# Kernel tuning notes

Measured on AMD Instinct MI355X. Metric: run time of the kernel, lower is better.

## Reference

```python
import jax, jax.numpy as jnp
import numpy as np

D_X, N_LAYERS, N_HEADS, D_OUT = 1024, 4, 16, 1024
D_H = D_X // N_HEADS
LN_EPS = 1e-5


def _layernorm(x, g, b):
    mu = jnp.mean(x, axis=-1, keepdims=True)
    var = jnp.var(x, axis=-1, keepdims=True)
    return (x - mu) * jax.lax.rsqrt(var + LN_EPS) * g + b


def setup_inputs() -> dict:
    key = jax.random.key(0)
    ks = jax.random.split(key, 12)
    s = 0.02
    inp = {
        "x": jax.random.normal(ks[0], (4, 1024, D_X), dtype=jnp.float32),
        # per-layer, per-head K/V projections (Q is unused by the original math)
        "Wk": jax.random.normal(ks[1], (N_LAYERS, N_HEADS, D_X, D_H), dtype=jnp.float32) * s,
        "bk": jnp.zeros((N_LAYERS, N_HEADS, D_H), dtype=jnp.float32),
        "Wv": jax.random.normal(ks[2], (N_LAYERS, N_HEADS, D_X, D_H), dtype=jnp.float32) * s,
        "bv": jnp.zeros((N_LAYERS, N_HEADS, D_H), dtype=jnp.float32),
        # per-layer FFN linear
        "Wl": jax.random.normal(ks[3], (N_LAYERS, D_X, D_X), dtype=jnp.float32) * s,
        "bl": jnp.zeros((N_LAYERS, D_X), dtype=jnp.float32),
        # per-layer LayerNorm params
        "g1": jnp.ones((N_LAYERS, D_X), dtype=jnp.float32),
        "b1": jnp.zeros((N_LAYERS, D_X), dtype=jnp.float32),
        "g2": jnp.ones((N_LAYERS, D_X), dtype=jnp.float32),
        "b2": jnp.zeros((N_LAYERS, D_X), dtype=jnp.float32),
        # output projection
        "Wo": jax.random.normal(ks[4], (D_X, D_OUT), dtype=jnp.float32) * s,
        "bo": jnp.zeros((D_OUT,), dtype=jnp.float32),
    }
    return inp


def reference(x, Wk, bk, Wv, bv, Wl, bl, g1, b1, g2, b2, Wo, bo):
    B, S, _ = x.shape
    scale = 1.0 / np.sqrt(D_H).astype(np.float32)
    for l in range(N_LAYERS):
        # batched across heads instead of the original per-head Python loop
        K = jnp.einsum("bsd,hdk->bhsk", x, Wk[l]) + bk[l][None, :, None, :]
        V = jnp.einsum("bsd,hdk->bhsk", x, Wv[l]) + bv[l][None, :, None, :]
        # faithful quirk: logits = K @ V^T (Q is never used in the source)
        logits = jnp.einsum("bhsk,bhtk->bhst", K, V) * scale
        attn = jnp.einsum("bhst,bhtk->bhsk", jax.nn.softmax(logits, axis=-1), V)
        attn = attn.transpose(0, 2, 1, 3).reshape(B, S, D_X)  # concat heads
        x = _layernorm(x + attn, g1[l], b1[l])
        ff = jax.nn.relu(jnp.einsum("bsd,de->bse", x, Wl[l]) + bl[l])
        x = _layernorm(x + ff, g2[l], b2[l])
    return jnp.einsum("bsd,do->bso", x, Wo) + bo
```

## Files before the change

### kernel.cpp

```cpp
#include <hip/hip_runtime.h>

typedef unsigned short u16;
typedef unsigned int u32;
typedef __attribute__((ext_vector_type(4))) float f32x4;
typedef __attribute__((ext_vector_type(8))) short short8;

#if __has_builtin(__builtin_amdgcn_exp2f)
#define EXP2(x) __builtin_amdgcn_exp2f(x)
#else
#define EXP2(x) exp2f(x)
#endif

#define SCALEK 0.18033688011112042f

__device__ __forceinline__ u16 f2b(float f) {
    unsigned u = __float_as_uint(f);
    u += 0x7fff + ((u >> 16) & 1);
    return (u16)(u >> 16);
}
__device__ __forceinline__ float b2f(u16 v) {
    return __uint_as_float(((unsigned)v) << 16);
}
__device__ __forceinline__ int swz(int byteoff) {
    return byteoff ^ (((byteoff >> 7) & 7) << 4);
}
__device__ __forceinline__ int swzV(int byteoff) {
    return byteoff ^ (((byteoff >> 8) & 7) << 4);
}
__device__ __forceinline__ void gl16(const u16* g, u16* l) {
    __builtin_amdgcn_global_load_lds(
        (const __attribute__((address_space(1))) unsigned*)(g),
        (__attribute__((address_space(3))) unsigned*)(l), 16, 0, 0);
}
__device__ __forceinline__ u32 cvtpk(float lo, float hi) {
    u32 r;
    asm("v_cvt_pk_bf16_f32 %0, %1, %2" : "=v"(r) : "v"(lo), "v"(hi));
    return r;
}
__device__ __forceinline__ void plswap(u32& a, u32& b) {
    asm("v_permlane32_swap_b32 %0, %1" : "+v"(a), "+v"(b));
    asm("v_permlane16_swap_b32 %0, %1" : "+v"(a), "+v"(b));
}
__device__ __forceinline__ void up8(uint4 u, float* v) {
    v[0] = b2f((u16)u.x); v[1] = b2f((u16)(u.x >> 16));
    v[2] = b2f((u16)u.y); v[3] = b2f((u16)(u.y >> 16));
    v[4] = b2f((u16)u.z); v[5] = b2f((u16)(u.z >> 16));
    v[6] = b2f((u16)u.w); v[7] = b2f((u16)(u.w >> 16));
}
#define MFMA16(a, b, c) __builtin_amdgcn_mfma_f32_16x16x32_bf16((a), (b), (c), 0, 0, 0)

__global__ __launch_bounds__(256) void pack_wkv_t(const float* __restrict__ W,
                                                  u16* __restrict__ out, int voff) {
    __shared__ float tile[32][33];
    int z = blockIdx.z; int l = z >> 4, h = z & 15;
    const float* ip = W + (size_t)z * 1024 * 64;
    u16* op = out + (size_t)l * 2048 * 1024 + (size_t)(voff + h * 64) * 1024;
    int tx = threadIdx.x & 31, ty = threadIdx.x >> 5;
    int d0 = blockIdx.y * 32, k0 = blockIdx.x * 32;
#pragma unroll
    for (int j = 0; j < 32; j += 8)
        tile[ty + j][tx] = ip[(size_t)(d0 + ty + j) * 64 + k0 + tx];
    __syncthreads();
#pragma unroll
    for (int j = 0; j < 32; j += 8)
        op[(size_t)(k0 + ty + j) * 1024 + d0 + tx] = f2b(tile[tx][ty + j]);
}

__global__ __launch_bounds__(256) void transpose_cvt(const float* __restrict__ in,
                                                     u16* __restrict__ out, int R, int C) {
    __shared__ float tile[32][33];
    const float* ip = in + (size_t)blockIdx.z * R * C;
    u16* op = out + (size_t)blockIdx.z * R * C;
    int tx = threadIdx.x & 31, ty = threadIdx.x >> 5;
    int r0 = blockIdx.y * 32, c0 = blockIdx.x * 32;
#pragma unroll
    for (int j = 0; j < 32; j += 8)
        tile[ty + j][tx] = ip[(size_t)(r0 + ty + j) * C + c0 + tx];
    __syncthreads();
#pragma unroll
    for (int j = 0; j < 32; j += 8)
        op[(size_t)(c0 + ty + j) * R + r0 + tx] = f2b(tile[tx][ty + j]);
}

__global__ __launch_bounds__(256) void cvt_bf16(const float* __restrict__ in,
                                                u16* __restrict__ out, int n) {
    int i = (blockIdx.x * 256 + threadIdx.x) * 4;
    if (i >= n) return;
    float4 v = *(const float4*)&in[i];
    ushort4 o = {f2b(v.x), f2b(v.y), f2b(v.z), f2b(v.w)};
    *(ushort4*)&out[i] = o;
}

template <int EPI, int BN>
__global__ __launch_bounds__(256) void gemm_bt(const u16* __restrict__ A,
                                               const u16* __restrict__ B,
                                               const float* __restrict__ bias1,
                                               const float* __restrict__ bias2, int split,
                                               void* __restrict__ Cv,
                                               u16* __restrict__ VTout,
                                               int M, int N, int K) {
    constexpr int NB = BN / 32;
    constexpr int NLB = BN / 32;
    constexpr int L2BN = (BN == 128) ? 7 : 6;
    __shared__ __align__(16) u16 lA[2][128 * 64];
    __shared__ __align__(16) u16 lB[2][BN * 64];
    const int t = threadIdx.x;
    const int lane = t & 63, w = t >> 6;
    const int wr = w >> 1, wc = w & 1;
    const int g = lane >> 4, r = lane & 15;
    const int bid = blockIdx.x;
    const int rgn = bid & 7, idx = bid >> 3;
    const int by = (rgn >> 1) * 8 + (idx >> 3);
    const int bx = (rgn & 1) * 8 + (idx & 7);
    const int m0 = by * 128, n0 = bx * BN;

    const u16* sA[4];
    const u16* sB[NLB];
#pragma unroll
    for (int j = 0; j < 4; ++j) {
        int c = j * 256 + t;
        sA[j] = A + (size_t)(m0 + (c & 127)) * K + (c >> 7) * 8;
    }
#pragma unroll
    for (int j = 0; j < NLB; ++j) {
        int c = j * 256 + t;
        sB[j] = B + (size_t)(n0 + (c & (BN - 1))) * K + (c >> L2BN) * 8;
    }

    f32x4 zero4 = {0.f, 0.f, 0.f, 0.f};
    f32x4 acc[4][NB];
#pragma unroll
    for (int m = 0; m < 4; ++m)
#pragma unroll
        for (int n = 0; n < NB; ++n) acc[m][n] = zero4;

#define GSTAGE(bufi, k0)                                                 \
    do {                                                                 \
        _Pragma("unroll") for (int j = 0; j < 4; ++j)                    \
            gl16(sA[j] + (k0), &lA[bufi][(j * 256 + w * 64) * 8]);       \
        _Pragma("unroll") for (int j = 0; j < NLB; ++j)                  \
            gl16(sB[j] + (k0), &lB[bufi][(j * 256 + w * 64) * 8]);       \
    } while (0)

    GSTAGE(0, 0);
    __syncthreads();
    const int nk = K >> 6;
    for (int kt = 0; kt < nk; ++kt) {
        const int cur = kt & 1;
        if (kt + 1 < nk) GSTAGE(cur ^ 1, (kt + 1) * 64);
#pragma unroll
        for (int ks = 0; ks < 2; ++ks) {
            short8 af[4], bf[NB];
#pragma unroll
            for (int m = 0; m < 4; ++m)
                af[m] = *(const short8*)&lA[cur][((ks * 4 + g) * 128 + wr * 64 + m * 16 + r) * 8];
#pragma unroll
            for (int n = 0; n < NB; ++n)
                bf[n] = *(const short8*)&lB[cur][((ks * 4 + g) * BN + wc * (BN / 2) + n * 16 + r) * 8];
#pragma unroll
            for (int m = 0; m < 4; ++m)
#pragma unroll
                for (int n = 0; n < NB; ++n)
                    acc[m][n] = MFMA16(af[m], bf[n], acc[m][n]);
        }
        __syncthreads();
    }
#undef GSTAGE

#pragma unroll
    for (int m = 0; m < 4; ++m) {
        int row = m0 + wr * 64 + m * 16 + g * 4;
#pragma unroll
        for (int n = 0; n < NB; ++n) {
            int col = n0 + wc * (BN / 2) + n * 16 + r;
            float bv_ = (col < split) ? bias1[col] : bias2[col - split];
            if (EPI == 0) {
                float sc = (col < split) ? SCALEK : 1.0f;
                ushort4 qv;
                qv.x = f2b((acc[m][n][0] + bv_) * sc);
                qv.y = f2b((acc[m][n][1] + bv_) * sc);
                qv.z = f2b((acc[m][n][2] + bv_) * sc);
                qv.w = f2b((acc[m][n][3] + bv_) * sc);
                u16* Cb = (u16*)Cv;
                Cb[(size_t)(row + 0) * N + col] = qv.x;
                Cb[(size_t)(row + 1) * N + col] = qv.y;
                Cb[(size_t)(row + 2) * N + col] = qv.z;
                Cb[(size_t)(row + 3) * N + col] = qv.w;
                if (col >= split) {
                    int d = col - split, b_ = row >> 10, s = row & 1023;
                    *(ushort4*)&VTout[(((size_t)(b_ * 16) + (d >> 6)) * 64 + (d & 63)) * 1024 + s] = qv;
                }
            } else if (EPI == 1) {
                u16* Cb = (u16*)Cv;
#pragma unroll
                for (int i = 0; i < 4; ++i)
                    Cb[(size_t)(row + i) * N + col] = f2b(fmaxf(acc[m][n][i] + bv_, 0.f));
            } else {
#pragma unroll
                for (int i = 0; i < 4; ++i)
                    ((float*)Cv)[(size_t)(row + i) * N + col] = acc[m][n][i] + bv_;
            }
        }
    }
}

__global__ __launch_bounds__(512) void attn_kernel(const u16* __restrict__ KV,
                                                   const u16* __restrict__ VT,
                                                   u16* __restrict__ Out) {
    __shared__ __align__(16) u16 kt[2][1024 * 8];
    __shared__ __align__(16) u16 vt[2][1024 * 8];
    const int t = threadIdx.x;
    const int lane = t & 63, w = t >> 6;
    const int g = lane >> 4, r = lane & 15;
    const int d0 = blockIdx.x;
    const int q = d0 >> 3;
    const int bh = (d0 & 7) * 8 + (q >> 3), qb = q & 7;
    const int h = bh & 15, b = bh >> 4;
    const u16* Kbase = KV + (size_t)b * 1024 * 2048 + h * 64;
    const u16* Vbase = Kbase + 1024;
    const u16* VTbase = VT + ((size_t)(b * 16 + h)) * 64 * 1024;

    const int qrow = qb * 128 + w * 16 + r;
    const short8 qf0 = *(const short8*)&Kbase[(size_t)qrow * 2048 + g * 8];
    const short8 qf1 = *(const short8*)&Kbase[(size_t)qrow * 2048 + 32 + g * 8];

    const int krow1 = t >> 3;
    const int kcol = ((((t & 7) * 16) ^ ((krow1 & 7) << 4)) >> 1);
    const u16* Ks1 = Vbase + (size_t)krow1 * 2048 + kcol;
    const u16* Ks2 = Vbase + (size_t)(64 + krow1) * 2048 + kcol;
    const int vrow1 = t >> 4;
    const int vcol = ((((t & 15) * 16) ^ ((vrow1 & 7) << 4)) >> 1);
    const u16* Vs1 = VTbase + (size_t)vrow1 * 1024 + vcol;
    const u16* Vs2 = VTbase + (size_t)(32 + vrow1) * 1024 + vcol;

#define STAGE(bufi, t0)                                              \
    do {                                                             \
        gl16(Ks1 + (size_t)(t0) * 2048, &kt[bufi][(w * 64) * 8]);    \
        gl16(Ks2 + (size_t)(t0) * 2048, &kt[bufi][(512 + w * 64) * 8]); \
        gl16(Vs1 + (t0), &vt[bufi][(w * 64) * 8]);                   \
        gl16(Vs2 + (t0), &vt[bufi][(512 + w * 64) * 8]);             \
    } while (0)

    STAGE(0, 0);

    float m = -1e30f, l = 0.f;
    f32x4 zero4 = {0.f, 0.f, 0.f, 0.f};
    f32x4 oacc[4];
#pragma unroll
    for (int n = 0; n < 4; ++n) oacc[n] = zero4;
    const int cbase = (lane & 48) | (g << 2);
    __syncthreads();

    for (int tt = 0; tt < 8; ++tt) {
        const int cur = tt & 1;
        if (tt < 7) STAGE(cur ^ 1, (tt + 1) * 128);
        const char* kbuf = (const char*)&kt[cur][0];
        const char* vbuf = (const char*)&vt[cur][0];

        f32x4 sfT[8];
#pragma unroll
        for (int n = 0; n < 8; ++n) sfT[n] = zero4;
        __builtin_amdgcn_s_setprio(1);
#pragma unroll
        for (int ks = 0; ks < 2; ++ks) {
            const short8 qf = ks ? qf1 : qf0;
#pragma unroll
            for (int n = 0; n < 8; ++n) {
                short8 kf = *(const short8*)(kbuf + swz((n * 16 + r) * 128 + ks * 64 + g * 16));
                sfT[n] = MFMA16(kf, qf, sfT[n]);
            }
        }
        __builtin_amdgcn_s_setprio(0);
        float rm = -1e30f;
#pragma unroll
        for (int n = 0; n < 8; ++n)
            rm = fmaxf(rm, fmaxf(fmaxf(sfT[n][0], sfT[n][1]), fmaxf(sfT[n][2], sfT[n][3])));
        rm = fmaxf(rm, __shfl_xor(rm, 16, 64));
        rm = fmaxf(rm, __shfl_xor(rm, 32, 64));
        if (!__all(rm <= m + 8.f)) {
            float mn = fmaxf(m, rm);
            float cc = EXP2(m - mn);
            m = mn;
            l *= cc;
#pragma unroll
            for (int i = 0; i < 4; ++i) {
                float ci = __shfl(cc, cbase + i, 64);
#pragma unroll
                for (int n = 0; n < 4; ++n) oacc[n][i] *= ci;
            }
        }
        float rs = 0.f;
#pragma unroll
        for (int n = 0; n < 8; ++n)
#pragma unroll
            for (int i = 0; i < 4; ++i) {
                float p = EXP2(sfT[n][i] - m);
                sfT[n][i] = p;
                rs += p;
            }
        rs += __shfl_xor(rs, 16, 64);
        rs += __shfl_xor(rs, 32, 64);
        l += rs;
        u32 wpk[8][2];
#pragma unroll
        for (int n = 0; n < 8; ++n) {
            wpk[n][0] = cvtpk(sfT[n][0], sfT[n][1]);
            wpk[n][1] = cvtpk(sfT[n][2], sfT[n][3]);
        }
        __builtin_amdgcn_s_setprio(1);
#pragma unroll
        for (int ks = 0; ks < 4; ++ks) {
            u32 a0 = wpk[2 * ks][0], a2 = wpk[2 * ks + 1][0];
            plswap(a0, a2);
            u32 a1 = wpk[2 * ks][1], a3 = wpk[2 * ks + 1][1];
            plswap(a1, a3);
            uint4 av;
            av.x = a0; av.y = a1; av.z = a2; av.w = a3;
            union { uint4 u; short8 s; } uc;
            uc.u = av;
            const short8 af = uc.s;
#pragma unroll
            for (int n = 0; n < 4; ++n) {
                short8 vf = *(const short8*)(vbuf + swzV((n * 16 + r) * 256 + ks * 64 + g * 16));
                oacc[n] = MFMA16(af, vf, oacc[n]);
            }
        }
        __builtin_amdgcn_s_setprio(0);
        __syncthreads();
    }
#undef STAGE

#pragma unroll
    for (int i = 0; i < 4; ++i) {
        float li = 1.f / __shfl(l, cbase + i, 64);
        int orow = b * 1024 + qb * 128 + w * 16 + g * 4 + i;
#pragma unroll
        for (int n = 0; n < 4; ++n)
            Out[(size_t)orow * 1024 + h * 64 + n * 16 + r] = f2b(oacc[n][i] * li);
    }
}

__global__ __launch_bounds__(256) void ln_kernel(const u16* __restrict__ xin,
                                                 const u16* __restrict__ addin,
                                                 const float* __restrict__ gamma,
                                                 const float* __restrict__ beta,
                                                 u16* __restrict__ xbout) {
    const int t = threadIdx.x, lane = t & 63, w = t >> 6;
    const int row = blockIdx.x * 4 + w;
    const size_t base = (size_t)row * 1024 + lane * 16;
    uint4 x0 = *(const uint4*)&xin[base];
    uint4 x1 = *(const uint4*)&xin[base + 8];
    uint4 a0 = *(const uint4*)&addin[base];
    uint4 a1 = *(const uint4*)&addin[base + 8];
    float v[16], av[16];
    up8(x0, v); up8(x1, v + 8);
    up8(a0, av); up8(a1, av + 8);
    float s = 0.f;
#pragma unroll
    for (int i = 0; i < 16; ++i) { v[i] += av[i]; s += v[i]; }
#pragma unroll
    for (int off = 32; off; off >>= 1) s += __shfl_xor(s, off, 64);
    const float mean = s * (1.f / 1024.f);
    float sq = 0.f;
#pragma unroll
    for (int i = 0; i < 16; ++i) { v[i] -= mean; sq += v[i] * v[i]; }
#pragma unroll
    for (int off = 32; off; off >>= 1) sq += __shfl_xor(sq, off, 64);
    const float rstd = rsqrtf(sq * (1.f / 1024.f) + 1e-5f);
    const float* gp = gamma + lane * 16;
    const float* bp = beta + lane * 16;
    u32 o[8];
#pragma unroll
    for (int j = 0; j < 8; ++j) {
        float o0 = v[2 * j] * rstd * gp[2 * j] + bp[2 * j];
        float o1 = v[2 * j + 1] * rstd * gp[2 * j + 1] + bp[2 * j + 1];
        o[j] = cvtpk(o0, o1);
    }
    uint4 w0 = {o[0], o[1], o[2], o[3]};
    uint4 w1 = {o[4], o[5], o[6], o[7]};
    *(uint4*)&xbout[base] = w0;
    *(uint4*)&xbout[base + 8] = w1;
}

extern "C" void kernel_launch(void* const* d_in, const int* in_sizes, int n_in,
                              void* d_out, int out_size, void* d_ws, size_t ws_size,
                              hipStream_t stream) {
    const float* x  = (const float*)d_in[0];
    const float* Wk = (const float*)d_in[1];
    const float* bk = (const float*)d_in[2];
    const float* Wv = (const float*)d_in[3];
    const float* bv = (const float*)d_in[4];
    const float* Wl = (const float*)d_in[5];
    const float* bl = (const float*)d_in[6];
    const float* g1 = (const float*)d_in[7];
    const float* b1 = (const float*)d_in[8];
    const float* g2 = (const float*)d_in[9];
    const float* b2 = (const float*)d_in[10];
    const float* Wo = (const float*)d_in[11];
    const float* bo = (const float*)d_in[12];

    char* ws = (char*)d_ws;
    u16* Wkvb = (u16*)ws;  ws += (size_t)4 * 2048 * 1024 * 2;
    u16* Wlb  = (u16*)ws;  ws += (size_t)4 * 1024 * 1024 * 2;
    u16* Wob  = (u16*)ws;  ws += (size_t)1024 * 1024 * 2;
    u16* xb   = (u16*)ws;  ws += (size_t)4096 * 1024 * 2;
    u16* KVb  = (u16*)ws;  ws += (size_t)4096 * 2048 * 2;
    u16* VTb  = (u16*)ws;  ws += (size_t)4096 * 1024 * 2;
    u16* tmpb = (u16*)ws;  ws += (size_t)4096 * 1024 * 2;

    pack_wkv_t<<<dim3(2, 32, 64), 256, 0, stream>>>(Wk, Wkvb, 0);
    pack_wkv_t<<<dim3(2, 32, 64), 256, 0, stream>>>(Wv, Wkvb, 1024);
    transpose_cvt<<<dim3(32, 32, 4), 256, 0, stream>>>(Wl, Wlb, 1024, 1024);
    transpose_cvt<<<dim3(32, 32, 1), 256, 0, stream>>>(Wo, Wob, 1024, 1024);
    cvt_bf16<<<dim3(4096), 256, 0, stream>>>(x, xb, 4096 * 1024);

    for (int l = 0; l < 4; ++l) {
        gemm_bt<0, 128><<<dim3(512), 256, 0, stream>>>(
            xb, Wkvb + (size_t)l * 2048 * 1024, bk + l * 1024, bv + l * 1024, 1024,
            (void*)KVb, VTb, 4096, 2048, 1024);
        attn_kernel<<<dim3(512), 512, 0, stream>>>(KVb, VTb, tmpb);
        ln_kernel<<<dim3(1024), 256, 0, stream>>>(
            xb, tmpb, g1 + l * 1024, b1 + l * 1024, xb);
        gemm_bt<1, 64><<<dim3(512), 256, 0, stream>>>(
            xb, Wlb + (size_t)l * 1024 * 1024, bl + l * 1024, bl + l * 1024, 1024,
            (void*)tmpb, nullptr, 4096, 1024, 1024);
        ln_kernel<<<dim3(1024), 256, 0, stream>>>(
            xb, tmpb, g2 + l * 1024, b2 + l * 1024, xb);
    }
    gemm_bt<2, 64><<<dim3(512), 256, 0, stream>>>(
        xb, Wob, bo, bo, 1024, d_out, nullptr, 4096, 1024, 1024);
}
```

Measured before the change: 498.1 us.

## Add 256x256-tile 8-wave ping-pong GEMM for fused K/V projection

Replaces the 128x128-tile K/V projection GEMM with a new 512-thread kernel that computes a 256x256 output tile per block. It interleaves direct global-to-LDS loads with MFMA clusters, using explicit barriers, s_waitcnt and setprio. The goals are more reuse of each loaded tile and overlap of memory traffic with matrix math. The cost is only 128 blocks on a GPU with 256 CUs, so many CUs sit idle, plus large register and LDS use per block. The old EPI==0 epilogue is removed from the generic GEMM.

```diff
diff --git a/kernel.cpp b/kernel.cpp
--- a/kernel.cpp
+++ b/kernel.cpp
@@ -89,6 +89,144 @@
     float4 v = *(const float4*)&in[i];
     ushort4 o = {f2b(v.x), f2b(v.y), f2b(v.z), f2b(v.w)};
     *(ushort4*)&out[i] = o;
+}
+
+__global__ __launch_bounds__(512, 2) void gemm8p(const u16* __restrict__ A,
+                                                 const u16* __restrict__ B,
+                                                 const float* __restrict__ bias1,
+                                                 const float* __restrict__ bias2,
+                                                 int split,
+                                                 u16* __restrict__ Cb,
+                                                 u16* __restrict__ VTout, int N) {
+    constexpr int K = 1024;
+    __shared__ __align__(16) u16 shA[2 * 2 * 8 * 128 * 8];
+    __shared__ __align__(16) u16 shB[2 * 2 * 8 * 128 * 8];
+    const int t = threadIdx.x;
+    const int lane = t & 63, w = t >> 6;
+    const int wrh = w >> 2;
+    const int wc3 = w & 3;
+    const int hb = wc3 >> 1;
+    const int rowb = (wc3 & 1) * 64;
+    const int g = lane >> 4, r = lane & 15;
+    const int bid = blockIdx.x;
+    const int bx = bid & 7, by = bid >> 3;
+    const int m0 = by * 256, n0 = bx * 256;
+
+    const int rowst = (w & 1) * 64 + lane;
+    const int kc1 = w >> 1;
+    const u16* aSrcB = A + (size_t)(m0 + rowst) * K + kc1 * 8;
+    const u16* bSrcB = B + (size_t)(n0 + rowst) * K + kc1 * 8;
+    u16* aD = shA + ((w >> 1) * 128 + (w & 1) * 64) * 8;
+    u16* bD = shB + ((w >> 1) * 128 + (w & 1) * 64) * 8;
+
+#define STG(DST, SRC, BUF, H, TAU)                                          \
+    do {                                                                    \
+        gl16((SRC) + (size_t)(H) * 128 * K + (TAU) * 64,                    \
+             (DST) + (((BUF) * 2 + (H)) * 8) * 128 * 8);                    \
+        gl16((SRC) + (size_t)(H) * 128 * K + (TAU) * 64 + 32,               \
+             (DST) + (((BUF) * 2 + (H)) * 8 + 4) * 128 * 8);                \
+    } while (0)
+
+    f32x4 zero4 = {0.f, 0.f, 0.f, 0.f};
+    f32x4 acc[8][4];
+#pragma unroll
+    for (int m = 0; m < 8; ++m)
+#pragma unroll
+        for (int n = 0; n < 4; ++n) acc[m][n] = zero4;
+
+    short8 af[2][4], bf[2][4];
+
+#define RDAF(BUF, MQ)                                                        \
+    _Pragma("unroll") for (int ks = 0; ks < 2; ++ks)                         \
+    _Pragma("unroll") for (int mm = 0; mm < 4; ++mm)                         \
+        af[ks][mm] = *(const short8*)&shA[((((BUF) * 2 + wrh) * 8 + ks * 4 + g) * 128 + (MQ) + mm * 16 + r) * 8];
+
+#define RDBF(BUF, NP)                                                        \
+    _Pragma("unroll") for (int ks = 0; ks < 2; ++ks)                         \
+    _Pragma("unroll") for (int nn = 0; nn < 2; ++nn)                         \
+        bf[ks][(NP) * 2 + nn] = *(const short8*)&shB[((((BUF) * 2 + hb) * 8 + ks * 4 + g) * 128 + rowb + (NP) * 32 + nn * 16 + r) * 8];
+
+#define CLUSTER(MQ, NP)                                                      \
+    __builtin_amdgcn_s_setprio(1);                                           \
+    _Pragma("unroll") for (int ks = 0; ks < 2; ++ks)                         \
+    _Pragma("unroll") for (int mm = 0; mm < 4; ++mm)                         \
+    _Pragma("unroll") for (int nn = 0; nn < 2; ++nn)                         \
+        acc[(MQ) + mm][(NP) * 2 + nn] =                                      \
+            MFMA16(af[ks][mm], bf[ks][(NP) * 2 + nn], acc[(MQ) + mm][(NP) * 2 + nn]); \
+    __builtin_amdgcn_s_setprio(0);
+
+#define BAR __builtin_amdgcn_s_barrier()
+
+    STG(aD, aSrcB, 0, 0, 0); STG(aD, aSrcB, 0, 1, 0);
+    STG(bD, bSrcB, 0, 0, 0); STG(bD, bSrcB, 0, 1, 0);
+    STG(bD, bSrcB, 1, 0, 1); STG(bD, bSrcB, 1, 1, 1);
+    asm volatile("s_waitcnt vmcnt(4)" ::: "memory");
+    __builtin_amdgcn_sched_barrier(0);
+    BAR;
+
+#pragma unroll 1
+    for (int it = 0; it < 8; ++it) {
+        const bool st2 = (it < 7);
+        STG(aD, aSrcB, 1, 0, 2 * it + 1);
+        RDAF(0, 0); RDBF(0, 0);
+        BAR; CLUSTER(0, 0); BAR;
+        STG(aD, aSrcB, 1, 1, 2 * it + 1);
+        RDBF(0, 1);
+        BAR; CLUSTER(0, 1); BAR;
+        if (st2) STG(bD, bSrcB, 0, 0, 2 * it + 2);
+        RDAF(0, 64);
+        BAR; CLUSTER(4, 0); BAR;
+        if (st2) STG(bD, bSrcB, 0, 1, 2 * it + 2);
+        BAR; CLUSTER(4, 1);
+        if (st2) { asm volatile("s_waitcnt vmcnt(4)" ::: "memory"); }
+        else     { asm volatile("s_waitcnt vmcnt(0)" ::: "memory"); }
+        __builtin_amdgcn_sched_barrier(0);
+        BAR;
+        if (st2) STG(aD, aSrcB, 0, 0, 2 * it + 2);
+        RDAF(1, 0); RDBF(1, 0);
+        BAR; CLUSTER(0, 0); BAR;
+        if (st2) STG(aD, aSrcB, 0, 1, 2 * it + 2);
+        RDBF(1, 1);
+        BAR; CLUSTER(0, 1); BAR;
+        if (st2) STG(bD, bSrcB, 1, 0, 2 * it + 3);
+        RDAF(1, 64);
+        BAR; CLUSTER(4, 0); BAR;
+        if (st2) STG(bD, bSrcB, 1, 1, 2 * it + 3);
+        BAR; CLUSTER(4, 1);
+        if (it < 6) { asm volatile("s_waitcnt vmcnt(4)" ::: "memory"); }
+        else        { asm volatile("s_waitcnt vmcnt(0)" ::: "memory"); }
+        __builtin_amdgcn_sched_barrier(0);
+        BAR;
+    }
+#undef STG
+#undef RDAF
+#undef RDBF
+#undef CLUSTER
+#undef BAR
+
+#pragma unroll
+    for (int m = 0; m < 8; ++m) {
+        int row = m0 + wrh * 128 + m * 16 + g * 4;
+#pragma unroll
+        for (int n = 0; n < 4; ++n) {
+            int col = n0 + wc3 * 64 + n * 16 + r;
+            float bv_ = (col < split) ? bias1[col] : bias2[col - split];
+            float sc = (col < split) ? SCALEK : 1.0f;
+            ushort4 qv;
+            qv.x = f2b((acc[m][n][0] + bv_) * sc);
+            qv.y = f2b((acc[m][n][1] + bv_) * sc);
+            qv.z = f2b((acc[m][n][2] + bv_) * sc);
+            qv.w = f2b((acc[m][n][3] + bv_) * sc);
+            Cb[(size_t)(row + 0) * N + col] = qv.x;
+            Cb[(size_t)(row + 1) * N + col] = qv.y;
+            Cb[(size_t)(row + 2) * N + col] = qv.z;
+            Cb[(size_t)(row + 3) * N + col] = qv.w;
+            if (col >= split) {
+                int d = col - split, b_ = row >> 10, s = row & 1023;
+                *(ushort4*)&VTout[(((size_t)(b_ * 16) + (d >> 6)) * 64 + (d & 63)) * 1024 + s] = qv;
+            }
+        }
+    }
 }
 
 template <int EPI, int BN>
@@ -174,23 +312,7 @@
         for (int n = 0; n < NB; ++n) {
             int col = n0 + wc * (BN / 2) + n * 16 + r;
             float bv_ = (col < split) ? bias1[col] : bias2[col - split];
-            if (EPI == 0) {
-                float sc = (col < split) ? SCALEK : 1.0f;
-                ushort4 qv;
-                qv.x = f2b((acc[m][n][0] + bv_) * sc);
-                qv.y = f2b((acc[m][n][1] + bv_) * sc);
-                qv.z = f2b((acc[m][n][2] + bv_) * sc);
-                qv.w = f2b((acc[m][n][3] + bv_) * sc);
-                u16* Cb = (u16*)Cv;
-                Cb[(size_t)(row + 0) * N + col] = qv.x;
-                Cb[(size_t)(row + 1) * N + col] = qv.y;
-                Cb[(size_t)(row + 2) * N + col] = qv.z;
-                Cb[(size_t)(row + 3) * N + col] = qv.w;
-                if (col >= split) {
-                    int d = col - split, b_ = row >> 10, s = row & 1023;
-                    *(ushort4*)&VTout[(((size_t)(b_ * 16) + (d >> 6)) * 64 + (d & 63)) * 1024 + s] = qv;
-                }
-            } else if (EPI == 1) {
+            if (EPI == 1) {
                 u16* Cb = (u16*)Cv;
 #pragma unroll
                 for (int i = 0; i < 4; ++i)
@@ -415,9 +537,9 @@
     cvt_bf16<<<dim3(4096), 256, 0, stream>>>(x, xb, 4096 * 1024);
 
     for (int l = 0; l < 4; ++l) {
-        gemm_bt<0, 128><<<dim3(512), 256, 0, stream>>>(
+        gemm8p<<<dim3(128), 512, 0, stream>>>(
             xb, Wkvb + (size_t)l * 2048 * 1024, bk + l * 1024, bv + l * 1024, 1024,
-            (void*)KVb, VTb, 4096, 2048, 1024);
+            KVb, VTb, 2048);
         attn_kernel<<<dim3(512), 512, 0, stream>>>(KVb, VTb, tmpb);
         ln_kernel<<<dim3(1024), 256, 0, stream>>>(
             xb, tmpb, g1 + l * 1024, b1 + l * 1024, xb);
```

New measurement: 557.5 us. +11.9%, slower.

## Add dedicated 256x128 KV-projection GEMM with fine-grained async staging pipeline

Applied to the files above, without the earlier changes.

Replaces the generic gemm_bt<0,128> for the K/V projection with a specialized 512-thread kernel using 256x128 tiles. Global-to-LDS loads are split into sub-stages interleaved with MFMA clusters, using explicit vmcnt waits, barriers and s_setprio, so memory traffic overlaps compute. Larger tiles reduce A/B refetch, but grid drops to 256 blocks at one block per CU, which may leave some CUs underused. The schedule hard-codes K=1024 and the tile grid.

```diff
diff --git a/kernel.cpp b/kernel.cpp
--- a/kernel.cpp
+++ b/kernel.cpp
@@ -89,6 +89,135 @@
     float4 v = *(const float4*)&in[i];
     ushort4 o = {f2b(v.x), f2b(v.y), f2b(v.z), f2b(v.w)};
     *(ushort4*)&out[i] = o;
+}
+
+__global__ __launch_bounds__(512, 1) void gemm_kv(const u16* __restrict__ A,
+                                                  const u16* __restrict__ B,
+                                                  const float* __restrict__ bias1,
+                                                  const float* __restrict__ bias2,
+                                                  int split,
+                                                  u16* __restrict__ Cb,
+                                                  u16* __restrict__ VTout, int N) {
+    constexpr int K = 1024;
+    __shared__ __align__(16) u16 shA[2 * 8 * 256 * 8];
+    __shared__ __align__(16) u16 shB[2 * 8 * 128 * 8];
+    const int t = threadIdx.x;
+    const int lane = t & 63, w = t >> 6;
+    const int wm = w >> 1, wn = w & 1;
+    const int g = lane >> 4, r = lane & 15;
+    const int bid = blockIdx.x;
+    const int bx = bid & 15, by = bid >> 4;
+    const int m0 = by * 256, n0 = bx * 128;
+
+    const u16* aS = A + (size_t)(m0 + (w & 3) * 64 + lane) * K + (w >> 2) * 8;
+    const u16* bS = B + (size_t)(n0 + (w & 1) * 64 + lane) * K + (w >> 1) * 8;
+
+#define STGA(BUF, U, TAU)                                                  \
+    gl16(aS + (TAU) * 64 + (U) * 16,                                       \
+         shA + (((BUF) * 8 + 2 * (U) + (w >> 2)) * 256 + (w & 3) * 64) * 8)
+#define STGB(BUF, U, TAU)                                                  \
+    gl16(bS + (TAU) * 64 + (U) * 32,                                       \
+         shB + (((BUF) * 8 + 4 * (U) + (w >> 1)) * 128 + (w & 1) * 64) * 8)
+
+    f32x4 zero4 = {0.f, 0.f, 0.f, 0.f};
+    f32x4 acc[4][4];
+#pragma unroll
+    for (int m = 0; m < 4; ++m)
+#pragma unroll
+        for (int n = 0; n < 4; ++n) acc[m][n] = zero4;
+
+    short8 af[2][2], bf[2][4];
+
+#define RDAF(BUF, MQ)                                                       \
+    _Pragma("unroll") for (int ks = 0; ks < 2; ++ks)                        \
+    _Pragma("unroll") for (int mm = 0; mm < 2; ++mm)                        \
+        af[ks][mm] = *(const short8*)&shA[((((BUF) * 8 + ks * 4 + g)) * 256 \
+            + wm * 64 + (MQ) * 32 + mm * 16 + r) * 8];
+#define RDBF(BUF)                                                           \
+    _Pragma("unroll") for (int ks = 0; ks < 2; ++ks)                        \
+    _Pragma("unroll") for (int nn = 0; nn < 4; ++nn)                        \
+        bf[ks][nn] = *(const short8*)&shB[((((BUF) * 8 + ks * 4 + g)) * 128 \
+            + wn * 64 + nn * 16 + r) * 8];
+#define CLUSTER(MQ)                                                         \
+    __builtin_amdgcn_s_setprio(1);                                          \
+    _Pragma("unroll") for (int ks = 0; ks < 2; ++ks)                        \
+    _Pragma("unroll") for (int mm = 0; mm < 2; ++mm)                        \
+    _Pragma("unroll") for (int nn = 0; nn < 4; ++nn)                        \
+        acc[(MQ) * 2 + mm][nn] =                                            \
+            MFMA16(af[ks][mm], bf[ks][nn], acc[(MQ) * 2 + mm][nn]);         \
+    __builtin_amdgcn_s_setprio(0);
+#define BAR __builtin_amdgcn_s_barrier()
+#define VMC(N)                                                              \
+    asm volatile("s_waitcnt vmcnt(%0)" :: "i"(N) : "memory");               \
+    __builtin_amdgcn_sched_barrier(0)
+
+    STGA(0, 0, 0); STGA(0, 1, 0); STGA(0, 2, 0); STGA(0, 3, 0);
+    STGB(0, 0, 0); STGB(0, 1, 0);
+    STGB(1, 0, 1); STGB(1, 1, 1);
+    VMC(2);
+    BAR;
+
+#pragma unroll 1
+    for (int it = 0; it < 8; ++it) {
+        const bool st = (it < 7);
+        const int t1 = 2 * it + 1, t2 = 2 * it + 2, t3 = 2 * it + 3;
+        STGA(1, 0, t1); STGA(1, 1, t1); STGA(1, 2, t1);
+        VMC(3);
+        BAR;
+        RDAF(0, 0); RDBF(0);
+        CLUSTER(0);
+        BAR;
+        STGA(1, 3, t1);
+        if (st) { STGB(0, 0, t2); STGB(0, 1, t2); }
+        if (st) { VMC(3); } else { VMC(1); }
+        BAR;
+        RDAF(0, 1);
+        CLUSTER(1);
+        BAR;
+        if (st) { STGA(0, 0, t2); STGA(0, 1, t2); STGA(0, 2, t2); }
+        if (st) { VMC(3); } else { VMC(1); }
+        BAR;
+        RDAF(1, 0); RDBF(1);
+        CLUSTER(0);
+        BAR;
+        if (st) { STGA(0, 3, t2); STGB(1, 0, t3); STGB(1, 1, t3); }
+        if (st) { VMC(3); } else { VMC(0); }
+        BAR;
+        RDAF(1, 1);
+        CLUSTER(1);
+        BAR;
+    }
+#undef STGA
+#undef STGB
+#undef RDAF
+#undef RDBF
+#undef CLUSTER
+#undef BAR
+#undef VMC
+
+#pragma unroll
+    for (int m = 0; m < 4; ++m) {
+        int row = m0 + wm * 64 + m * 16 + g * 4;
+#pragma unroll
+        for (int n = 0; n < 4; ++n) {
+            int col = n0 + wn * 64 + n * 16 + r;
+            float bv_ = (col < split) ? bias1[col] : bias2[col - split];
+            float sc = (col < split) ? SCALEK : 1.0f;
+            ushort4 qv;
+            qv.x = f2b((acc[m][n][0] + bv_) * sc);
+            qv.y = f2b((acc[m][n][1] + bv_) * sc);
+            qv.z = f2b((acc[m][n][2] + bv_) * sc);
+            qv.w = f2b((acc[m][n][3] + bv_) * sc);
+            Cb[(size_t)(row + 0) * N + col] = qv.x;
+            Cb[(size_t)(row + 1) * N + col] = qv.y;
+            Cb[(size_t)(row + 2) * N + col] = qv.z;
+            Cb[(size_t)(row + 3) * N + col] = qv.w;
+            if (col >= split) {
+                int d = col - split, b_ = row >> 10, s = row & 1023;
+                *(ushort4*)&VTout[(((size_t)(b_ * 16) + (d >> 6)) * 64 + (d & 63)) * 1024 + s] = qv;
+            }
+        }
+    }
 }
 
 template <int EPI, int BN>
@@ -174,23 +303,7 @@
         for (int n = 0; n < NB; ++n) {
             int col = n0 + wc * (BN / 2) + n * 16 + r;
             float bv_ = (col < split) ? bias1[col] : bias2[col - split];
-            if (EPI == 0) {
-                float sc = (col < split) ? SCALEK : 1.0f;
-                ushort4 qv;
-                qv.x = f2b((acc[m][n][0] + bv_) * sc);
-                qv.y = f2b((acc[m][n][1] + bv_) * sc);
-                qv.z = f2b((acc[m][n][2] + bv_) * sc);
-                qv.w = f2b((acc[m][n][3] + bv_) * sc);
-                u16* Cb = (u16*)Cv;
-                Cb[(size_t)(row + 0) * N + col] = qv.x;
-                Cb[(size_t)(row + 1) * N + col] = qv.y;
-                Cb[(size_t)(row + 2) * N + col] = qv.z;
-                Cb[(size_t)(row + 3) * N + col] = qv.w;
-                if (col >= split) {
-                    int d = col - split, b_ = row >> 10, s = row & 1023;
-                    *(ushort4*)&VTout[(((size_t)(b_ * 16) + (d >> 6)) * 64 + (d & 63)) * 1024 + s] = qv;
-                }
-            } else if (EPI == 1) {
+            if (EPI == 1) {
                 u16* Cb = (u16*)Cv;
 #pragma unroll
                 for (int i = 0; i < 4; ++i)
@@ -415,9 +528,9 @@
     cvt_bf16<<<dim3(4096), 256, 0, stream>>>(x, xb, 4096 * 1024);
 
     for (int l = 0; l < 4; ++l) {
-        gemm_bt<0, 128><<<dim3(512), 256, 0, stream>>>(
+        gemm_kv<<<dim3(256), 512, 0, stream>>>(
             xb, Wkvb + (size_t)l * 2048 * 1024, bk + l * 1024, bv + l * 1024, 1024,
-            (void*)KVb, VTb, 4096, 2048, 1024);
+            KVb, VTb, 2048);
         attn_kernel<<<dim3(512), 512, 0, stream>>>(KVb, VTb, tmpb);
         ln_kernel<<<dim3(1024), 256, 0, stream>>>(
             xb, tmpb, g1 + l * 1024, b1 + l * 1024, xb);
```

New measurement: 515.0 us. 1.03x slower.
